# Kernel tuning notes

Measured on AMD Instinct MI355X. Metric: run time of the kernel, lower is better.

## Reference

```python
import jax, jax.numpy as jnp
import numpy as np

N_NODES = 100000
N_EDGES = 1600000
IN_DIM = 128
HID = 64
N_CLASSES = 40
NEG_SLOPE = 0.2


def setup_inputs() -> dict:
    key = jax.random.key(0)
    ks = jax.random.split(key, 12)
    s_in = 1.0 / np.sqrt(IN_DIM)
    s_h = 1.0 / np.sqrt(HID)
    return {
        "x": jax.random.normal(ks[0], (N_NODES, IN_DIM), dtype=jnp.float32),
        "edge_index": jax.random.randint(ks[1], (2, N_EDGES), 0, N_NODES, dtype=jnp.int64),
        "W0": jax.random.normal(ks[2], (IN_DIM, HID), dtype=jnp.float32) * s_in,
        "a_s0": jax.random.normal(ks[3], (HID,), dtype=jnp.float32) * s_h,
        "a_d0": jax.random.normal(ks[4], (HID,), dtype=jnp.float32) * s_h,
        "b0": jnp.zeros((HID,), dtype=jnp.float32),
        "W1": jax.random.normal(ks[5], (HID, HID), dtype=jnp.float32) * s_h,
        "a_s1": jax.random.normal(ks[6], (HID,), dtype=jnp.float32) * s_h,
        "a_d1": jax.random.normal(ks[7], (HID,), dtype=jnp.float32) * s_h,
        "b1": jnp.zeros((HID,), dtype=jnp.float32),
        "Wl": jax.random.normal(ks[8], (HID, N_CLASSES), dtype=jnp.float32) * s_h,
        "bl": jnp.zeros((N_CLASSES,), dtype=jnp.float32),
    }


def gat_conv(x, src, dst, W, a_s, a_d, b, n_nodes):
    # single-head GATConv (PyG default heads=1), self-loops already in src/dst
    h = x @ W                                  # [N, d]
    e = jax.nn.leaky_relu((h @ a_s)[src] + (h @ a_d)[dst], NEG_SLOPE)  # [E]
    # segment softmax over incoming edges of each dst node
    m = jax.ops.segment_max(e, dst, num_segments=n_nodes)
    p = jnp.exp(e - m[dst])
    denom = jax.ops.segment_sum(p, dst, num_segments=n_nodes)
    alpha = p / (denom[dst] + 1e-16)           # [E]
    out = jax.ops.segment_sum(alpha[:, None] * h[src], dst, num_segments=n_nodes)
    return out + b


def reference(x, edge_index, W0, a_s0, a_d0, b0, W1, a_s1, a_d1, b1, Wl, bl):
    n = x.shape[0]
    loop = jnp.arange(n, dtype=edge_index.dtype)
    src = jnp.concatenate([edge_index[0], loop])
    dst = jnp.concatenate([edge_index[1], loop])
    h = gat_conv(x, src, dst, W0, a_s0, a_d0, b0, n)
    h = jax.nn.elu(h)
    h = gat_conv(h, src, dst, W1, a_s1, a_d1, b1, n)
    h = jax.nn.elu(h)
    return h @ Wl + bl
```

## Files before the change

kernel.cpp:

```cpp
#include <hip/hip_runtime.h>
#include <math.h>

#define NEG_SLOPE 0.2f
#define CAP 256
#define BSH 9
#define BSZ 512
#define CHUNK 4096
#define PADS 16
#define CAPQ 16384
#define CAPB 10240

typedef __attribute__((ext_vector_type(8))) short short8;
typedef __attribute__((ext_vector_type(4))) float f32x4;

__device__ __forceinline__ float hred_sum(float v) {
#pragma unroll
    for (int o = 16; o >= 1; o >>= 1) v += __shfl_xor(v, o, 64);
    return v;
}
__device__ __forceinline__ unsigned int f2bf(float f) {
    unsigned int u = __float_as_uint(f);
    return (u + 0x7fffu + ((u >> 16) & 1u)) >> 16;
}
__device__ __forceinline__ float bflo(unsigned int u) { return __uint_as_float(u << 16); }
__device__ __forceinline__ float bfhi(unsigned int u) { return __uint_as_float(u & 0xffff0000u); }


__device__ __forceinline__ void scatter_body(char* smem, int bid,
        const int* __restrict__ src, const int* __restrict__ dst,
        int* __restrict__ bcursor, int* __restrict__ ebuf, int E) {
    int* lh = (int*)smem;
    int* lb = lh + 256;
    const int tid = threadIdx.x;
    int base = bid * CHUNK;
    int sv[16], dv[16];
    bool ok[16];
#pragma unroll
    for (int u = 0; u < 16; ++u) {
        int i = base + u * 256 + tid;
        ok[u] = i < E;
        int ii = ok[u] ? i : E - 1;
        dv[u] = dst[ii];
        sv[u] = src[ii];
    }
    lh[tid] = 0;
    __syncthreads();
#pragma unroll
    for (int u = 0; u < 16; ++u)
        if (ok[u]) atomicAdd(&lh[dv[u] >> BSH], 1);
    __syncthreads();
    int c = lh[tid];
    lb[tid] = c ? atomicAdd(&bcursor[tid * PADS], c) : 0;
    lh[tid] = 0;
    __syncthreads();
#pragma unroll
    for (int u = 0; u < 16; ++u) {
        if (ok[u]) {
            int d = dv[u], b = d >> BSH;
            int pp = atomicAdd(&lh[b], 1);
            int pos = lb[b] + pp;
            if (pos < CAPQ)
                ebuf[b * CAPQ + pos] = (sv[u] << BSH) | (d & (BSZ - 1));
        }
    }
}

__device__ __forceinline__ void gemm0_body(char* smem, int bid,
        const float* __restrict__ X, const float* __restrict__ W,
        const float* __restrict__ a_s, const float* __restrict__ a_d,
        unsigned int* __restrict__ hb, float* __restrict__ ss, float* __restrict__ sd, int N) {
    constexpr int K = 128, OUTW = 64, NKC = K / 32, NC = OUTW / 16;
    short* wfrag = (short*)smem;
    unsigned int* hs = (unsigned int*)(smem + NKC * NC * 64 * 8 * 2);

    const int tid  = threadIdx.x;
    const int lane = tid & 63;
    const int w    = tid >> 6;
    const int m    = lane & 15;
    const int q8   = lane >> 4;
    const int rowbase = bid * 64 + w * 16;

    for (int f = tid; f < NKC * NC * 64; f += 256) {
        int flane = f & 63;
        int fc    = (f >> 6) % NC;
        int fkc   = (f >> 6) / NC;
        int col   = fc * 16 + (flane & 15);
        int k0    = fkc * 32 + (flane >> 4) * 8;
        short8 b;
#pragma unroll
        for (int j = 0; j < 8; ++j) b[j] = (short)f2bf(W[(k0 + j) * OUTW + col]);
        *(short8*)&wfrag[f * 8] = b;
    }
    __syncthreads();

    int grow = rowbase + m; if (grow >= N) grow = N - 1;

    f32x4 acc[NC];
#pragma unroll
    for (int c = 0; c < NC; ++c) acc[c] = (f32x4)0.f;

    const float* xrow = X + (size_t)grow * K + q8 * 8;
#pragma unroll
    for (int kc = 0; kc < NKC; ++kc) {
        float4 v0 = *(const float4*)(xrow + kc * 32);
        float4 v1 = *(const float4*)(xrow + kc * 32 + 4);
        float vv[8] = {v0.x, v0.y, v0.z, v0.w, v1.x, v1.y, v1.z, v1.w};
        short8 ah, al;
#pragma unroll
        for (int j = 0; j < 8; ++j) {
            unsigned int hb16 = f2bf(vv[j]);
            ah[j] = (short)hb16;
            al[j] = (short)f2bf(vv[j] - __uint_as_float(hb16 << 16));
        }
#pragma unroll
        for (int c = 0; c < NC; ++c) {
            short8 b = *(short8*)&wfrag[((kc * NC + c) * 64 + lane) * 8];
            acc[c] = __builtin_amdgcn_mfma_f32_16x16x32_bf16(ah, b, acc[c], 0, 0, 0);
            acc[c] = __builtin_amdgcn_mfma_f32_16x16x32_bf16(al, b, acc[c], 0, 0, 0);
        }
    }

    float asv[NC], adv[NC];
#pragma unroll
    for (int c = 0; c < NC; ++c) { asv[c] = a_s[c * 16 + m]; adv[c] = a_d[c * 16 + m]; }
#pragma unroll
    for (int i = 0; i < 4; ++i) {
        float s = 0.f, d = 0.f;
#pragma unroll
        for (int c = 0; c < NC; ++c) {
            s = fmaf(acc[c][i], asv[c], s);
            d = fmaf(acc[c][i], adv[c], d);
        }
#pragma unroll
        for (int o = 1; o <= 8; o <<= 1) {
            s += __shfl_xor(s, o, 64);
            d += __shfl_xor(d, o, 64);
        }
        int r = rowbase + q8 * 4 + i;
        if (m == 0 && r < N) { ss[r] = s; sd[r] = d; }
    }

    unsigned short* hsw = (unsigned short*)&hs[w * 512];
#pragma unroll
    for (int c = 0; c < NC; ++c)
#pragma unroll
        for (int i = 0; i < 4; ++i)
            hsw[(q8 * 4 + i) * 64 + c * 16 + m] = (unsigned short)f2bf(acc[c][i]);
    unsigned int* hu = &hs[w * 512];
    int row = lane >> 2, u0 = (lane & 3) * 8;
    uint4 va = *(uint4*)&hu[row * 32 + u0];
    uint4 vb = *(uint4*)&hu[row * 32 + u0 + 4];
    int r = rowbase + row;
    if (r < N) {
        *(uint4*)&hb[(size_t)r * 32 + u0]     = va;
        *(uint4*)&hb[(size_t)r * 32 + u0 + 4] = vb;
    }
}

__global__ __launch_bounds__(256) void k_scatter_gemm0(
        const int* __restrict__ src, const int* __restrict__ dst,
        int* __restrict__ bcursor, int* __restrict__ ebuf, int E, int nscat,
        const float* __restrict__ X, const float* __restrict__ W,
        const float* __restrict__ a_s, const float* __restrict__ a_d,
        unsigned int* __restrict__ hb, float* __restrict__ ss, float* __restrict__ sd, int N) {
    __shared__ __align__(16) char smem[24576];
    if ((int)blockIdx.x < nscat)
        scatter_body(smem, blockIdx.x, src, dst, bcursor, ebuf, E);
    else
        gemm0_body(smem, blockIdx.x - nscat, X, W, a_s, a_d, hb, ss, sd, N);
}


__global__ __launch_bounds__(1024) void k_build(const int* __restrict__ bcursor,
                                                const int* __restrict__ ebuf,
                                                int* __restrict__ rowptr, int* __restrict__ csr,
                                                int N, int nbuck) {
    __shared__ int sdeg[BSZ], sscan[BSZ];
    __shared__ int sebuf[CAPB];
    __shared__ int shdr[2];
    int b = blockIdx.x, t = threadIdx.x;
    int nlo = b << BSH;
    int cn = N - nlo; if (cn > BSZ) cn = BSZ;

    int bcv = 0, totv = 0;
    if (t < 256) {
        int cnb = 0;
        if (t < nbuck) {
            bcv = bcursor[t * PADS]; if (bcv > CAPQ) bcv = CAPQ;
            cnb = N - (t << BSH); if (cnb > BSZ) cnb = BSZ; if (cnb < 0) cnb = 0;
        }
        totv = bcv + cnb;
        sscan[t] = totv;
    }
    __syncthreads();
#pragma unroll
    for (int off = 1; off < 256; off <<= 1) {
        int u = 0;
        if (t < 256 && t >= off) u = sscan[t - off];
        __syncthreads();
        if (t < 256) sscan[t] += u;
        __syncthreads();
    }
    if (t == b) { shdr[0] = sscan[t] - totv; shdr[1] = bcv; }
    if (b == 0 && t == nbuck - 1) rowptr[N] = sscan[t];
    __syncthreads();
    int cb = shdr[0], ec = shdr[1];
    int e0 = b * CAPQ;

    if (t < BSZ) sdeg[t] = (t < cn) ? 1 : 0;
    __syncthreads();
    int ecl = ec < CAPB ? ec : CAPB;
    {
        int i = t;
        for (; i + 3 * 1024 < ecl; i += 4 * 1024) {
            int r0 = ebuf[e0 + i],        r1 = ebuf[e0 + i + 1024];
            int r2 = ebuf[e0 + i + 2048], r3 = ebuf[e0 + i + 3072];
            sebuf[i] = r0; sebuf[i + 1024] = r1; sebuf[i + 2048] = r2; sebuf[i + 3072] = r3;
            atomicAdd(&sdeg[r0 & (BSZ - 1)], 1);
            atomicAdd(&sdeg[r1 & (BSZ - 1)], 1);
            atomicAdd(&sdeg[r2 & (BSZ - 1)], 1);
            atomicAdd(&sdeg[r3 & (BSZ - 1)], 1);
        }
        for (; i < ecl; i += 1024) {
            int r = ebuf[e0 + i];
            sebuf[i] = r;
            atomicAdd(&sdeg[r & (BSZ - 1)], 1);
        }
        for (i = CAPB + t; i < ec; i += 1024)
            atomicAdd(&sdeg[ebuf[e0 + i] & (BSZ - 1)], 1);
    }
    __syncthreads();
    int v = 0;
    if (t < BSZ) { v = sdeg[t]; sscan[t] = v; }
    __syncthreads();
#pragma unroll
    for (int off = 1; off < BSZ; off <<= 1) {
        int u = 0;
        if (t < BSZ && t >= off) u = sscan[t - off];
        __syncthreads();
        if (t < BSZ) sscan[t] += u;
        __syncthreads();
    }
    if (t < BSZ) {
        int excl = sscan[t] - v;
        if (t < cn) {
            rowptr[nlo + t] = cb + excl;
            csr[cb + excl] = nlo + t;
            sdeg[t] = excl + 1;
        }
    }
    __syncthreads();
    {
        int i = t;
        for (; i + 3 * 1024 < ecl; i += 4 * 1024) {
            int r0 = sebuf[i],        r1 = sebuf[i + 1024];
            int r2 = sebuf[i + 2048], r3 = sebuf[i + 3072];
            int p0 = atomicAdd(&sdeg[r0 & (BSZ - 1)], 1);
            int p1 = atomicAdd(&sdeg[r1 & (BSZ - 1)], 1);
            int p2 = atomicAdd(&sdeg[r2 & (BSZ - 1)], 1);
            int p3 = atomicAdd(&sdeg[r3 & (BSZ - 1)], 1);
            csr[cb + p0] = r0 >> BSH;
            csr[cb + p1] = r1 >> BSH;
            csr[cb + p2] = r2 >> BSH;
            csr[cb + p3] = r3 >> BSH;
        }
        for (; i < ecl; i += 1024) {
            int rec = sebuf[i];
            int p = atomicAdd(&sdeg[rec & (BSZ - 1)], 1);
            csr[cb + p] = rec >> BSH;
        }
        for (i = CAPB + t; i < ec; i += 1024) {
            int rec = ebuf[e0 + i];
            int p = atomicAdd(&sdeg[rec & (BSZ - 1)], 1);
            csr[cb + p] = rec >> BSH;
        }
    }
}


template <int K, int OUTW, bool SS, bool HB, bool XB>
__global__ __launch_bounds__(256) void k_gemm(const void* __restrict__ X,
                                              const float* __restrict__ W,
                                              const float* __restrict__ a_s,
                                              const float* __restrict__ a_d,
                                              const float* __restrict__ bias,
                                              void* __restrict__ Hout,
                                              float* __restrict__ ss,
                                              float* __restrict__ sd, int N) {
    constexpr int NKC = K / 32;
    constexpr int NC  = (OUTW + 15) / 16;
    __shared__ __align__(16) short wfrag[NKC * NC * 64 * 8];
    __shared__ __align__(16) unsigned int hs[HB ? 4 : 1][16 * 32];

    const int tid  = threadIdx.x;
    const int lane = tid & 63;
    const int w    = tid >> 6;
    const int m    = lane & 15;
    const int q8   = lane >> 4;
    const int rowbase = blockIdx.x * 64 + w * 16;

    for (int f = tid; f < NKC * NC * 64; f += 256) {
        int flane = f & 63;
        int fc    = (f >> 6) % NC;
        int fkc   = (f >> 6) / NC;
        int col   = fc * 16 + (flane & 15);
        int k0    = fkc * 32 + (flane >> 4) * 8;
        short8 b;
#pragma unroll
        for (int j = 0; j < 8; ++j) {
            float v = (col < OUTW) ? W[(k0 + j) * OUTW + col] : 0.f;
            b[j] = (short)f2bf(v);
        }
        *(short8*)&wfrag[f * 8] = b;
    }
    __syncthreads();

    int grow = rowbase + m; if (grow >= N) grow = N - 1;

    f32x4 acc[NC];
#pragma unroll
    for (int c = 0; c < NC; ++c) acc[c] = (f32x4)0.f;

    if (XB) {
        const unsigned short* xrow = (const unsigned short*)X + (size_t)grow * 64 + q8 * 8;
#pragma unroll
        for (int kc = 0; kc < NKC; ++kc) {
            short8 ah = *(const short8*)(xrow + kc * 32);
#pragma unroll
            for (int c = 0; c < NC; ++c) {
                short8 b = *(short8*)&wfrag[((kc * NC + c) * 64 + lane) * 8];
                acc[c] = __builtin_amdgcn_mfma_f32_16x16x32_bf16(ah, b, acc[c], 0, 0, 0);
            }
        }
    } else {
        const float* xrow = (const float*)X + (size_t)grow * K + q8 * 8;
#pragma unroll
        for (int kc = 0; kc < NKC; ++kc) {
            float4 v0 = *(const float4*)(xrow + kc * 32);
            float4 v1 = *(const float4*)(xrow + kc * 32 + 4);
            float vv[8] = {v0.x, v0.y, v0.z, v0.w, v1.x, v1.y, v1.z, v1.w};
            short8 ah, al;
#pragma unroll
            for (int j = 0; j < 8; ++j) {
                unsigned int hb16 = f2bf(vv[j]);
                ah[j] = (short)hb16;
                al[j] = (short)f2bf(vv[j] - __uint_as_float(hb16 << 16));
            }
#pragma unroll
            for (int c = 0; c < NC; ++c) {
                short8 b = *(short8*)&wfrag[((kc * NC + c) * 64 + lane) * 8];
                acc[c] = __builtin_amdgcn_mfma_f32_16x16x32_bf16(ah, b, acc[c], 0, 0, 0);
                acc[c] = __builtin_amdgcn_mfma_f32_16x16x32_bf16(al, b, acc[c], 0, 0, 0);
            }
        }
    }

    if (SS) {
        float asv[NC], adv[NC];
#pragma unroll
        for (int c = 0; c < NC; ++c) { asv[c] = a_s[c * 16 + m]; adv[c] = a_d[c * 16 + m]; }
#pragma unroll
        for (int i = 0; i < 4; ++i) {
            float s = 0.f, d = 0.f;
#pragma unroll
            for (int c = 0; c < NC; ++c) {
                s = fmaf(acc[c][i], asv[c], s);
                d = fmaf(acc[c][i], adv[c], d);
            }
#pragma unroll
            for (int o = 1; o <= 8; o <<= 1) {
                s += __shfl_xor(s, o, 64);
                d += __shfl_xor(d, o, 64);
            }
            int r = rowbase + q8 * 4 + i;
            if (m == 0 && r < N) { ss[r] = s; sd[r] = d; }
        }
    }

    if (HB) {
        unsigned short* hsw = (unsigned short*)&hs[w][0];
#pragma unroll
        for (int c = 0; c < NC; ++c)
#pragma unroll
            for (int i = 0; i < 4; ++i)
                hsw[(q8 * 4 + i) * 64 + c * 16 + m] = (unsigned short)f2bf(acc[c][i]);
        unsigned int* hu = &hs[w][0];
        int row = lane >> 2, u0 = (lane & 3) * 8;
        uint4 va = *(uint4*)&hu[row * 32 + u0];
        uint4 vb = *(uint4*)&hu[row * 32 + u0 + 4];
        int r = rowbase + row;
        if (r < N) {
            unsigned int* hbp = (unsigned int*)Hout;
            *(uint4*)&hbp[(size_t)r * 32 + u0]     = va;
            *(uint4*)&hbp[(size_t)r * 32 + u0 + 4] = vb;
        }
    } else {
        float bv[NC];
#pragma unroll
        for (int c = 0; c < NC; ++c) {
            int col = c * 16 + m;
            bv[c] = (col < OUTW) ? bias[col] : 0.f;
        }
        float* O = (float*)Hout;
#pragma unroll
        for (int i = 0; i < 4; ++i) {
            int r = rowbase + q8 * 4 + i;
            if (r < N) {
#pragma unroll
                for (int c = 0; c < NC; ++c) {
                    int col = c * 16 + m;
                    if (col < OUTW) O[(size_t)r * OUTW + col] = acc[c][i] + bv[c];
                }
            }
        }
    }
}


__global__ __launch_bounds__(256) void k_agg(const int* __restrict__ rowptr, const int* __restrict__ csr,
                                             const float* __restrict__ ss, const float* __restrict__ sd,
                                             const unsigned int* __restrict__ hb, const float* __restrict__ bias,
                                             unsigned int* __restrict__ z, int N) {
    __shared__ __align__(16) float sal[8][CAP];
    __shared__ __align__(16) int   sof[8][CAP];
    const int tid = threadIdx.x;
    const int hw  = tid >> 5;
    const int p   = tid & 31;
    const int n   = blockIdx.x * 8 + hw;
    const bool valid = n < N;
    const char* hbb = (const char*)hb;
    const int p4 = p * 4;

    int ro = 0, deg = 0;
    float sdn = 0.f;
    if (valid) {
        ro  = rowptr[n];
        deg = rowptr[n + 1] - ro;
        sdn = sd[n];
    }

    if (deg <= CAP) {
        float sum = 0.f;
        for (int j = p; j < deg; j += 32) {
            int s = csr[ro + j];
            float e = ss[s] + sdn;
            e = fmaxf(e, NEG_SLOPE * e);
            float pe = __expf(e);
            sal[hw][j] = pe;
            sof[hw][j] = s << 7;
            sum += pe;
        }
        sum = hred_sum(sum);
        float inv = 1.f / (sum + 1e-16f);

        float ax = 0.f, ay = 0.f, bx = 0.f, by = 0.f, cx = 0.f, cy = 0.f, dx = 0.f, dy = 0.f;
        int j = 0;
        for (; j + 7 < deg; j += 8) {
            float4 al0 = *(const float4*)&sal[hw][j];
            float4 al1 = *(const float4*)&sal[hw][j + 4];
            int4   of0 = *(const int4*)&sof[hw][j];
            int4   of1 = *(const int4*)&sof[hw][j + 4];
            unsigned int u0 = *(const unsigned int*)(hbb + (of0.x + p4));
            unsigned int u1 = *(const unsigned int*)(hbb + (of0.y + p4));
            unsigned int u2 = *(const unsigned int*)(hbb + (of0.z + p4));
            unsigned int u3 = *(const unsigned int*)(hbb + (of0.w + p4));
            unsigned int u4 = *(const unsigned int*)(hbb + (of1.x + p4));
            unsigned int u5 = *(const unsigned int*)(hbb + (of1.y + p4));
            unsigned int u6 = *(const unsigned int*)(hbb + (of1.z + p4));
            unsigned int u7 = *(const unsigned int*)(hbb + (of1.w + p4));
            ax = fmaf(bflo(u0), al0.x, ax); ay = fmaf(bfhi(u0), al0.x, ay);
            bx = fmaf(bflo(u1), al0.y, bx); by = fmaf(bfhi(u1), al0.y, by);
            cx = fmaf(bflo(u2), al0.z, cx); cy = fmaf(bfhi(u2), al0.z, cy);
            dx = fmaf(bflo(u3), al0.w, dx); dy = fmaf(bfhi(u3), al0.w, dy);
            ax = fmaf(bflo(u4), al1.x, ax); ay = fmaf(bfhi(u4), al1.x, ay);
            bx = fmaf(bflo(u5), al1.y, bx); by = fmaf(bfhi(u5), al1.y, by);
            cx = fmaf(bflo(u6), al1.z, cx); cy = fmaf(bfhi(u6), al1.z, cy);
            dx = fmaf(bflo(u7), al1.w, dx); dy = fmaf(bfhi(u7), al1.w, dy);
        }
        for (; j + 3 < deg; j += 4) {
            float4 al0 = *(const float4*)&sal[hw][j];
            int4   of0 = *(const int4*)&sof[hw][j];
            unsigned int u0 = *(const unsigned int*)(hbb + (of0.x + p4));
            unsigned int u1 = *(const unsigned int*)(hbb + (of0.y + p4));
            unsigned int u2 = *(const unsigned int*)(hbb + (of0.z + p4));
            unsigned int u3 = *(const unsigned int*)(hbb + (of0.w + p4));
            ax = fmaf(bflo(u0), al0.x, ax); ay = fmaf(bfhi(u0), al0.x, ay);
            bx = fmaf(bflo(u1), al0.y, bx); by = fmaf(bfhi(u1), al0.y, by);
            cx = fmaf(bflo(u2), al0.z, cx); cy = fmaf(bfhi(u2), al0.z, cy);
            dx = fmaf(bflo(u3), al0.w, dx); dy = fmaf(bfhi(u3), al0.w, dy);
        }
        for (; j < deg; ++j) {
            float a = sal[hw][j];
            unsigned int u0 = *(const unsigned int*)(hbb + (sof[hw][j] + p4));
            ax = fmaf(bflo(u0), a, ax); ay = fmaf(bfhi(u0), a, ay);
        }
        float fx = (ax + bx) + (cx + dx);
        float fy = (ay + by) + (cy + dy);
        if (valid) {
            float2 ob = *(const float2*)&bias[p * 2];
            float ox = fmaf(fx, inv, ob.x);
            float oy = fmaf(fy, inv, ob.y);
            ox = (ox > 0.f) ? ox : __expf(ox) - 1.f;
            oy = (oy > 0.f) ? oy : __expf(oy) - 1.f;
            z[(size_t)n * 32 + p] = (f2bf(oy) << 16) | f2bf(ox);
        }
    } else {
        float sum = 0.f;
        for (int j = p; j < deg; j += 32) {
            int s = csr[ro + j];
            float e = ss[s] + sdn;
            e = fmaxf(e, NEG_SLOPE * e);
            sum += __expf(e);
        }
        sum = hred_sum(sum);
        float inv = 1.f / (sum + 1e-16f);
        float fx = 0.f, fy = 0.f;
        for (int j = 0; j < deg; ++j) {
            int s = csr[ro + j];
            float e = ss[s] + sdn;
            e = fmaxf(e, NEG_SLOPE * e);
            float pe = __expf(e);
            unsigned int u = *(const unsigned int*)(hbb + ((s << 7) + p4));
            fx = fmaf(bflo(u), pe, fx); fy = fmaf(bfhi(u), pe, fy);
        }
        float2 ob = *(const float2*)&bias[p * 2];
        float ox = fmaf(fx, inv, ob.x);
        float oy = fmaf(fy, inv, ob.y);
        ox = (ox > 0.f) ? ox : __expf(ox) - 1.f;
        oy = (oy > 0.f) ? oy : __expf(oy) - 1.f;
        z[(size_t)n * 32 + p] = (f2bf(oy) << 16) | f2bf(ox);
    }
}


extern "C" void kernel_launch(void* const* d_in, const int* in_sizes, int n_in,
                              void* d_out, int out_size, void* d_ws, size_t ws_size,
                              hipStream_t stream) {
    const float* x   = (const float*)d_in[0];
    const int*   ei  = (const int*)d_in[1];
    const float* W0  = (const float*)d_in[2];
    const float* as0 = (const float*)d_in[3];
    const float* ad0 = (const float*)d_in[4];
    const float* b0  = (const float*)d_in[5];
    const float* W1  = (const float*)d_in[6];
    const float* as1 = (const float*)d_in[7];
    const float* ad1 = (const float*)d_in[8];
    const float* b1  = (const float*)d_in[9];
    const float* Wl  = (const float*)d_in[10];
    const float* bl  = (const float*)d_in[11];
    float* out = (float*)d_out;

    int N = in_sizes[0] / 128;
    int E = in_sizes[1] / 2;
    const int* srcp = ei;
    const int* dstp = ei + E;
    int nbuck = (N + BSZ - 1) >> BSH;

    char* wp = (char*)d_ws;
    auto alloc = [&](size_t bytes) { void* p = (void*)wp; wp += (bytes + 255) & ~(size_t)255; return p; };
    unsigned int* hb = (unsigned int*)alloc((size_t)N * 32 * 4);
    unsigned int* z  = (unsigned int*)alloc((size_t)N * 32 * 4);
    float* ssb     = (float*)alloc((size_t)N * 4);
    float* sdb     = (float*)alloc((size_t)N * 4);
    int*   rowptr  = (int*)alloc((size_t)(N + 1) * 4);
    int*   csr     = (int*)alloc((size_t)(E + N) * 4);
    int*   ebuf    = (int*)alloc((size_t)nbuck * CAPQ * 4);
    int*   bcursor = (int*)alloc(256 * PADS * 4);

    int nscat = (E + CHUNK - 1) / CHUNK;
    int gb = (N + 63) / 64;

    hipMemsetAsync(bcursor, 0, 256 * PADS * 4, stream);
    k_scatter_gemm0<<<nscat + gb, 256, 0, stream>>>(srcp, dstp, bcursor, ebuf, E, nscat,
                                                    x, W0, as0, ad0, hb, ssb, sdb, N);
    k_build<<<nbuck, 1024, 0, stream>>>(bcursor, ebuf, rowptr, csr, N, nbuck);

    k_agg<<<(N + 7) / 8, 256, 0, stream>>>(rowptr, csr, ssb, sdb, hb, b0, z, N);
    k_gemm<64, 64, true, true, true><<<gb, 256, 0, stream>>>(z, W1, as1, ad1, nullptr, hb, ssb, sdb, N);
    k_agg<<<(N + 7) / 8, 256, 0, stream>>>(rowptr, csr, ssb, sdb, hb, b1, z, N);
    k_gemm<64, 40, false, false, true><<<gb, 256, 0, stream>>>(z, Wl, nullptr, nullptr, bl, out, nullptr, nullptr, N);
}
```

Baseline: 243.9 us.

## Co-schedule layer-0 GEMM with CSR build instead of with edge scatter

Splits the scatter out into its own kernel and fuses the first-layer GEMM with the CSR build into one 512-thread kernel, so the GEMM overlaps with the build phase instead of with the scatter. The build no longer stages bucket records in a large shared buffer and rereads them from global memory in the second pass. This cuts the shared-memory footprint and raises occupancy. GEMM blocks now cover 128 rows with 8 waves. The trade-off is a second global read of the edge buckets.

```diff
diff --git a/kernel.cpp b/kernel.cpp
--- a/kernel.cpp
+++ b/kernel.cpp
@@ -8,7 +8,6 @@
 #define CHUNK 4096
 #define PADS 16
 #define CAPQ 16384
-#define CAPB 10240
 
 typedef __attribute__((ext_vector_type(8))) short short8;
 typedef __attribute__((ext_vector_type(4))) float f32x4;
@@ -26,13 +25,12 @@
 __device__ __forceinline__ float bfhi(unsigned int u) { return __uint_as_float(u & 0xffff0000u); }
 
 
-__device__ __forceinline__ void scatter_body(char* smem, int bid,
+__global__ __launch_bounds__(256) void k_scatter(
         const int* __restrict__ src, const int* __restrict__ dst,
         int* __restrict__ bcursor, int* __restrict__ ebuf, int E) {
-    int* lh = (int*)smem;
-    int* lb = lh + 256;
+    __shared__ int lh[256], lb[256];
     const int tid = threadIdx.x;
-    int base = bid * CHUNK;
+    int base = blockIdx.x * CHUNK;
     int sv[16], dv[16];
     bool ok[16];
 #pragma unroll
@@ -65,22 +63,23 @@
     }
 }
 
+
 __device__ __forceinline__ void gemm0_body(char* smem, int bid,
         const float* __restrict__ X, const float* __restrict__ W,
         const float* __restrict__ a_s, const float* __restrict__ a_d,
         unsigned int* __restrict__ hb, float* __restrict__ ss, float* __restrict__ sd, int N) {
     constexpr int K = 128, OUTW = 64, NKC = K / 32, NC = OUTW / 16;
     short* wfrag = (short*)smem;
-    unsigned int* hs = (unsigned int*)(smem + NKC * NC * 64 * 8 * 2);
+    unsigned int* hs = (unsigned int*)(smem + 16384);
 
     const int tid  = threadIdx.x;
     const int lane = tid & 63;
     const int w    = tid >> 6;
     const int m    = lane & 15;
     const int q8   = lane >> 4;
-    const int rowbase = bid * 64 + w * 16;
-
-    for (int f = tid; f < NKC * NC * 64; f += 256) {
+    const int rowbase = bid * 128 + w * 16;
+
+    for (int f = tid; f < NKC * NC * 64; f += 512) {
         int flane = f & 63;
         int fc    = (f >> 6) % NC;
         int fkc   = (f >> 6) / NC;
@@ -157,28 +156,15 @@
     }
 }
 
-__global__ __launch_bounds__(256) void k_scatter_gemm0(
-        const int* __restrict__ src, const int* __restrict__ dst,
-        int* __restrict__ bcursor, int* __restrict__ ebuf, int E, int nscat,
-        const float* __restrict__ X, const float* __restrict__ W,
-        const float* __restrict__ a_s, const float* __restrict__ a_d,
-        unsigned int* __restrict__ hb, float* __restrict__ ss, float* __restrict__ sd, int N) {
-    __shared__ __align__(16) char smem[24576];
-    if ((int)blockIdx.x < nscat)
-        scatter_body(smem, blockIdx.x, src, dst, bcursor, ebuf, E);
-    else
-        gemm0_body(smem, blockIdx.x - nscat, X, W, a_s, a_d, hb, ss, sd, N);
-}
-
-
-__global__ __launch_bounds__(1024) void k_build(const int* __restrict__ bcursor,
-                                                const int* __restrict__ ebuf,
-                                                int* __restrict__ rowptr, int* __restrict__ csr,
-                                                int N, int nbuck) {
-    __shared__ int sdeg[BSZ], sscan[BSZ];
-    __shared__ int sebuf[CAPB];
-    __shared__ int shdr[2];
-    int b = blockIdx.x, t = threadIdx.x;
+__device__ __forceinline__ void build_body(char* smem, int b,
+        const int* __restrict__ bcursor, const int* __restrict__ ebuf,
+        int* __restrict__ rowptr, int* __restrict__ csr,
+        int N, int nbuck) {
+    int* sdeg  = (int*)smem;
+    int* sscan = sdeg + 512;
+    int* shdr  = sscan + 512;
+    const int t = threadIdx.x;
+
     int nlo = b << BSH;
     int cn = N - nlo; if (cn > BSZ) cn = BSZ;
 
@@ -207,54 +193,44 @@
     int cb = shdr[0], ec = shdr[1];
     int e0 = b * CAPQ;
 
-    if (t < BSZ) sdeg[t] = (t < cn) ? 1 : 0;
-    __syncthreads();
-    int ecl = ec < CAPB ? ec : CAPB;
+    sdeg[t] = (t < cn) ? 1 : 0;
+    __syncthreads();
     {
         int i = t;
-        for (; i + 3 * 1024 < ecl; i += 4 * 1024) {
-            int r0 = ebuf[e0 + i],        r1 = ebuf[e0 + i + 1024];
-            int r2 = ebuf[e0 + i + 2048], r3 = ebuf[e0 + i + 3072];
-            sebuf[i] = r0; sebuf[i + 1024] = r1; sebuf[i + 2048] = r2; sebuf[i + 3072] = r3;
+        for (; i + 1536 < ec; i += 2048) {
+            int r0 = ebuf[e0 + i], r1 = ebuf[e0 + i + 512];
+            int r2 = ebuf[e0 + i + 1024], r3 = ebuf[e0 + i + 1536];
             atomicAdd(&sdeg[r0 & (BSZ - 1)], 1);
             atomicAdd(&sdeg[r1 & (BSZ - 1)], 1);
             atomicAdd(&sdeg[r2 & (BSZ - 1)], 1);
             atomicAdd(&sdeg[r3 & (BSZ - 1)], 1);
         }
-        for (; i < ecl; i += 1024) {
-            int r = ebuf[e0 + i];
-            sebuf[i] = r;
-            atomicAdd(&sdeg[r & (BSZ - 1)], 1);
-        }
-        for (i = CAPB + t; i < ec; i += 1024)
+        for (; i < ec; i += 512)
             atomicAdd(&sdeg[ebuf[e0 + i] & (BSZ - 1)], 1);
     }
     __syncthreads();
-    int v = 0;
-    if (t < BSZ) { v = sdeg[t]; sscan[t] = v; }
+    int v = sdeg[t];
+    sscan[t] = v;
     __syncthreads();
 #pragma unroll
     for (int off = 1; off < BSZ; off <<= 1) {
-        int u = 0;
-        if (t < BSZ && t >= off) u = sscan[t - off];
+        int u = (t >= off) ? sscan[t - off] : 0;
         __syncthreads();
-        if (t < BSZ) sscan[t] += u;
+        sscan[t] += u;
         __syncthreads();
     }
-    if (t < BSZ) {
-        int excl = sscan[t] - v;
-        if (t < cn) {
-            rowptr[nlo + t] = cb + excl;
-            csr[cb + excl] = nlo + t;
-            sdeg[t] = excl + 1;
-        }
+    int excl = sscan[t] - v;
+    if (t < cn) {
+        rowptr[nlo + t] = cb + excl;
+        csr[cb + excl] = nlo + t;
+        sdeg[t] = excl + 1;
     }
     __syncthreads();
     {
         int i = t;
-        for (; i + 3 * 1024 < ecl; i += 4 * 1024) {
-            int r0 = sebuf[i],        r1 = sebuf[i + 1024];
-            int r2 = sebuf[i + 2048], r3 = sebuf[i + 3072];
+        for (; i + 1536 < ec; i += 2048) {
+            int r0 = ebuf[e0 + i], r1 = ebuf[e0 + i + 512];
+            int r2 = ebuf[e0 + i + 1024], r3 = ebuf[e0 + i + 1536];
             int p0 = atomicAdd(&sdeg[r0 & (BSZ - 1)], 1);
             int p1 = atomicAdd(&sdeg[r1 & (BSZ - 1)], 1);
             int p2 = atomicAdd(&sdeg[r2 & (BSZ - 1)], 1);
@@ -264,17 +240,26 @@
             csr[cb + p2] = r2 >> BSH;
             csr[cb + p3] = r3 >> BSH;
         }
-        for (; i < ecl; i += 1024) {
-            int rec = sebuf[i];
-            int p = atomicAdd(&sdeg[rec & (BSZ - 1)], 1);
-            csr[cb + p] = rec >> BSH;
-        }
-        for (i = CAPB + t; i < ec; i += 1024) {
+        for (; i < ec; i += 512) {
             int rec = ebuf[e0 + i];
             int p = atomicAdd(&sdeg[rec & (BSZ - 1)], 1);
             csr[cb + p] = rec >> BSH;
         }
     }
+}
+
+__global__ __launch_bounds__(512) void k_mid(
+        int* __restrict__ bcursor, int* __restrict__ ebuf, int gbm, int nbuck,
+        const float* __restrict__ X, const float* __restrict__ W,
+        const float* __restrict__ a_s, const float* __restrict__ a_d,
+        unsigned int* __restrict__ hb, float* __restrict__ ss, float* __restrict__ sd,
+        int* __restrict__ rowptr, int* __restrict__ csr, int N) {
+    __shared__ __align__(16) char smem[32768];
+    int bid = blockIdx.x;
+    if (bid < gbm)
+        gemm0_body(smem, bid, X, W, a_s, a_d, hb, ss, sd, N);
+    else
+        build_body(smem, bid - gbm, bcursor, ebuf, rowptr, csr, N, nbuck);
 }
 
 
@@ -568,15 +553,17 @@
     int*   bcursor = (int*)alloc(256 * PADS * 4);
 
     int nscat = (E + CHUNK - 1) / CHUNK;
-    int gb = (N + 63) / 64;
+    int gbm = (N + 127) / 128;
+    int gb2 = (N + 63) / 64;
 
     hipMemsetAsync(bcursor, 0, 256 * PADS * 4, stream);
-    k_scatter_gemm0<<<nscat + gb, 256, 0, stream>>>(srcp, dstp, bcursor, ebuf, E, nscat,
-                                                    x, W0, as0, ad0, hb, ssb, sdb, N);
-    k_build<<<nbuck, 1024, 0, stream>>>(bcursor, ebuf, rowptr, csr, N, nbuck);
+    k_scatter<<<nscat, 256, 0, stream>>>(srcp, dstp, bcursor, ebuf, E);
+    k_mid<<<gbm + nbuck, 512, 0, stream>>>(bcursor, ebuf, gbm, nbuck,
+                                           x, W0, as0, ad0, hb, ssb, sdb,
+                                           rowptr, csr, N);
 
     k_agg<<<(N + 7) / 8, 256, 0, stream>>>(rowptr, csr, ssb, sdb, hb, b0, z, N);
-    k_gemm<64, 64, true, true, true><<<gb, 256, 0, stream>>>(z, W1, as1, ad1, nullptr, hb, ssb, sdb, N);
+    k_gemm<64, 64, true, true, true><<<gb2, 256, 0, stream>>>(z, W1, as1, ad1, nullptr, hb, ssb, sdb, N);
     k_agg<<<(N + 7) / 8, 256, 0, stream>>>(rowptr, csr, ssb, sdb, hb, b1, z, N);
-    k_gemm<64, 40, false, false, true><<<gb, 256, 0, stream>>>(z, Wl, nullptr, nullptr, bl, out, nullptr, nullptr, N);
-}
+    k_gemm<64, 40, false, false, true><<<gb2, 256, 0, stream>>>(z, Wl, nullptr, nullptr, bl, out, nullptr, nullptr, N);
+}
```

Measured after the change: 239.9 us. Within noise of the previous version (-1.6%).
